# Optimization experiments

Measured on AMD Instinct MI355X. Metric: run time of the kernel, lower is better.

Reference implementation:

```python
import jax, jax.numpy as jnp
import numpy as np

B, L, H, U = 4, 4096, 1024, 1024


def setup_inputs() -> dict:
    key = jax.random.key(0)
    k0, k1, k2, k3 = jax.random.split(key, 4)
    inputs = jax.random.normal(k0, (B, L, H), dtype=jnp.float32)
    # linear layer params (torch default init scale ~ 1/sqrt(fan_in))
    W_rkv = jax.random.normal(k1, (H, 3 * U), dtype=jnp.float32) / np.sqrt(H)
    b_rkv = jnp.zeros((3 * U,), dtype=jnp.float32)
    W_o = jax.random.normal(k2, (U, H), dtype=jnp.float32) / np.sqrt(U)
    b_o = jnp.zeros((H,), dtype=jnp.float32)
    # nu_log init exactly as in the torch module
    r_min, r_max = 0.9, 0.999
    u = jax.random.uniform(k3, (U,), dtype=jnp.float32)
    nu_log = jnp.log(-0.5 * jnp.log(u * (r_max ** 2 - r_min ** 2) + r_min ** 2))
    gamma_log = jnp.zeros((U,), dtype=jnp.float32)
    return {"inputs": inputs, "W_rkv": W_rkv, "b_rkv": b_rkv,
            "W_o": W_o, "b_o": b_o, "nu_log": nu_log, "gamma_log": gamma_log}


def reference(inputs, W_rkv, b_rkv, W_o, b_o, nu_log, gamma_log):
    # projections
    rkv = jnp.einsum('blh,hu->blu', inputs, W_rkv) + b_rkv  # [B,L,3U]
    r, k, v = jnp.split(rkv, 3, axis=-1)
    r = jax.nn.sigmoid(r)
    k = jnp.exp(k)
    kv = k * v
    u = jnp.concatenate([kv, k], axis=-1)                   # [B,L,2U]
    nu = jnp.exp(jnp.concatenate([nu_log, nu_log]))         # [2U]
    gamma = jnp.exp(nu_log + gamma_log) - 1.0               # [U]
    lam = jnp.exp(-nu)                                      # per-channel decay
    # The torch log-depth doubling scan computes the linear recurrence
    # y_t = lam * y_{t-1} + u_t (y_0 = u_0). Use an associative scan over L.
    a = jnp.broadcast_to(lam, u.shape)

    def combine(c1, c2):
        a1, x1 = c1
        a2, x2 = c2
        return (a1 * a2, x1 * a2 + x2)

    _, y = jax.lax.associative_scan(combine, (a, u), axis=1)  # [B,L,2U]
    u1, u2 = jnp.split(y, 2, axis=-1)
    x = (u1 + gamma * kv) / (u2 + gamma * k + 1e-6) * r       # [B,L,U]
    return jnp.einsum('blu,uh->blh', x, W_o) + b_o
```

## Files before the change

kernel.cpp:

```cpp
#include <hip/hip_runtime.h>
#include <hip/hip_bf16.h>
#include <cstdint>
#include <cstddef>

constexpr int NB = 4;
constexpr int NL = 4096;
constexpr int NH = 1024;
constexpr int NU = 1024;
constexpr int NM = NB * NL;
constexpr int NCHUNK = 32;
constexpr int CLEN = NL / NCHUNK;

typedef __bf16 bf16x8 __attribute__((ext_vector_type(8)));
typedef __bf16 bf16x4 __attribute__((ext_vector_type(4)));
typedef float  f32x4  __attribute__((ext_vector_type(4)));

__global__ __launch_bounds__(256) void cast_f32_to_bf16(
    const float* __restrict__ in, __bf16* __restrict__ out, int n4) {
  int stride = gridDim.x * 256;
  for (int i = blockIdx.x * 256 + threadIdx.x; i < n4; i += stride) {
    const float4 v = reinterpret_cast<const float4*>(in)[i];
    bf16x4 o;
    o[0] = (__bf16)v.x; o[1] = (__bf16)v.y; o[2] = (__bf16)v.z; o[3] = (__bf16)v.w;
    reinterpret_cast<bf16x4*>(out)[i] = o;
  }
}

__global__ __launch_bounds__(256) void transpose_cast(
    const float* __restrict__ W, __bf16* __restrict__ Wt, int K, int N) {
  __shared__ float tile[32][33];
  int tx = threadIdx.x, ty = threadIdx.y;
  int n0 = blockIdx.x * 32, k0 = blockIdx.y * 32;
  #pragma unroll
  for (int i = 0; i < 32; i += 8)
    tile[ty + i][tx] = W[(size_t)(k0 + ty + i) * N + n0 + tx];
  __syncthreads();
  #pragma unroll
  for (int i = 0; i < 32; i += 8)
    Wt[(size_t)(n0 + ty + i) * K + k0 + tx] = (__bf16)tile[tx][ty + i];
}


#define SBAR0 __builtin_amdgcn_sched_barrier(0)

template<int EPI>
__global__ __launch_bounds__(512, 2) void gemm256(
    const __bf16* __restrict__ A, const __bf16* __restrict__ Bt,
    int M, int N, int K,
    const float* __restrict__ bias,
    float* __restrict__ out_r, float* __restrict__ out_k, float* __restrict__ out_v,
    float* __restrict__ out_f32) {
  __shared__ __attribute__((aligned(16))) __bf16 sA[2][256 * 64];
  __shared__ __attribute__((aligned(16))) __bf16 sB[2][256 * 64];

  const int tid = threadIdx.x;
  const int lane = tid & 63;
  const int w = tid >> 6;
  const int wm = w >> 2, wn = w & 3;

  const int ntn = N >> 8;
  const int nwg = gridDim.x;
  const int bid = blockIdx.x;
  const int cpx = nwg >> 3;
  const int swz = (bid & 7) * cpx + (bid >> 3);
  const int mt = swz / ntn, nt = swz % ntn;
  const long m0 = (long)mt * 256;
  const long n0 = (long)nt * 256;
  const int KT = K >> 6;

  const int srow = lane >> 3;
  const int scol = ((lane & 7) ^ srow) << 4;

  auto stageA = [&](int bi, int qm, int t) {
    if (t >= KT) return;
    #pragma unroll
    for (int j = 0; j < 2; ++j) {
      int u = w * 2 + j;
      int row0 = (u < 8) ? (qm * 64 + u * 8) : (128 + qm * 64 + (u - 8) * 8);
      const char* src = (const char*)A + ((m0 + row0 + srow) * (long)K + (long)t * 64) * 2 + scol;
      __builtin_amdgcn_global_load_lds(
          (const __attribute__((address_space(1))) unsigned int*)src,
          (__attribute__((address_space(3))) unsigned int*)((char*)&sA[bi][0] + row0 * 128),
          16, 0, 0);
    }
  };
  auto stageB = [&](int bi, int qn, int t) {
    if (t >= KT) return;
    #pragma unroll
    for (int j = 0; j < 2; ++j) {
      int u = w * 2 + j;
      int row0 = (u >> 2) * 64 + qn * 32 + (u & 3) * 8;
      const char* src = (const char*)Bt + ((n0 + row0 + srow) * (long)K + (long)t * 64) * 2 + scol;
      __builtin_amdgcn_global_load_lds(
          (const __attribute__((address_space(1))) unsigned int*)src,
          (__attribute__((address_space(3))) unsigned int*)((char*)&sB[bi][0] + row0 * 128),
          16, 0, 0);
    }
  };

  f32x4 acc[8][4];
  #pragma unroll
  for (int i = 0; i < 8; ++i)
    #pragma unroll
    for (int j = 0; j < 4; ++j) acc[i][j] = (f32x4)0.f;

#define PHASE(QM, QN, STAGE_STMT)                                              \
  do {                                                                         \
    const char* sAb = (const char*)&sA[bi][0];                                 \
    const char* sBb = (const char*)&sB[bi][0];                                 \
    bf16x8 av[4][2], bv[2][2];                                                 \
    _Pragma("unroll")                                                          \
    for (int f = 0; f < 4; ++f) {                                              \
      _Pragma("unroll")                                                        \
      for (int ks = 0; ks < 2; ++ks) {                                         \
        int r = wm * 128 + ((QM) * 4 + f) * 16 + (lane & 15);                  \
        int c = ks * 64 + (lane & 48);                                         \
        av[f][ks] = *(const bf16x8*)(sAb + r * 128 + (c ^ ((r & 7) << 4)));    \
      }                                                                        \
    }                                                                          \
    _Pragma("unroll")                                                          \
    for (int g = 0; g < 2; ++g) {                                              \
      _Pragma("unroll")                                                        \
      for (int ks = 0; ks < 2; ++ks) {                                         \
        int r = wn * 64 + ((QN) * 2 + g) * 16 + (lane & 15);                   \
        int c = ks * 64 + (lane & 48);                                         \
        bv[g][ks] = *(const bf16x8*)(sBb + r * 128 + (c ^ ((r & 7) << 4)));    \
      }                                                                        \
    }                                                                          \
    STAGE_STMT;                                                                \
    SBAR0;                                                                     \
    __builtin_amdgcn_s_barrier();                                              \
    SBAR0;                                                                     \
    __builtin_amdgcn_s_setprio(1);                                             \
    _Pragma("unroll")                                                          \
    for (int f = 0; f < 4; ++f) {                                              \
      _Pragma("unroll")                                                        \
      for (int g = 0; g < 2; ++g) {                                            \
        acc[(QM) * 4 + f][(QN) * 2 + g] = __builtin_amdgcn_mfma_f32_16x16x32_bf16( \
            av[f][0], bv[g][0], acc[(QM) * 4 + f][(QN) * 2 + g], 0, 0, 0);     \
        acc[(QM) * 4 + f][(QN) * 2 + g] = __builtin_amdgcn_mfma_f32_16x16x32_bf16( \
            av[f][1], bv[g][1], acc[(QM) * 4 + f][(QN) * 2 + g], 0, 0, 0);     \
      }                                                                        \
    }                                                                          \
    __builtin_amdgcn_s_setprio(0);                                             \
    SBAR0;                                                                     \
  } while (0)

#define EBAR { __builtin_amdgcn_s_barrier(); SBAR0; }

  stageA(0, 0, 0); stageB(0, 0, 0); stageA(0, 1, 0); stageB(0, 1, 0);
  stageA(1, 0, 1); stageB(1, 0, 1);
  SBAR0;
  asm volatile("s_waitcnt vmcnt(4)" ::: "memory");
  EBAR;

  for (int t = 0; t < KT; ++t) {
    const int bi = t & 1;
    PHASE(0, 0, stageB(bi ^ 1, 1, t + 1)); EBAR;
    PHASE(1, 0, stageA(bi ^ 1, 1, t + 1)); EBAR;
    PHASE(0, 1, stageB(bi, 0, t + 2));     EBAR;
    PHASE(1, 1, stageA(bi, 0, t + 2));
    SBAR0;
    if (t < KT - 2) { asm volatile("s_waitcnt vmcnt(4)" ::: "memory"); }
    else            { asm volatile("s_waitcnt vmcnt(0)" ::: "memory"); }
    EBAR;
  }
#undef PHASE
#undef EBAR

  float bs[4];
  #pragma unroll
  for (int fn = 0; fn < 4; ++fn)
    bs[fn] = bias[n0 + wn * 64 + fn * 16 + (lane & 15)];

  #pragma unroll
  for (int fm = 0; fm < 8; ++fm) {
    #pragma unroll
    for (int fn = 0; fn < 4; ++fn) {
      #pragma unroll
      for (int rr = 0; rr < 4; ++rr) {
        long row = m0 + wm * 128 + fm * 16 + (lane >> 4) * 4 + rr;
        long col = n0 + wn * 64 + fn * 16 + (lane & 15);
        float val = acc[fm][fn][rr] + bs[fn];
        if constexpr (EPI == 0) {
          int reg = (int)(col >> 10);
          int u = (int)(col & 1023);
          size_t idx = (size_t)row * NU + u;
          if (reg == 0)      out_r[idx] = 1.f / (1.f + __expf(-val));
          else if (reg == 1) out_k[idx] = __expf(val);
          else               out_v[idx] = val;
        } else {
          out_f32[(size_t)row * N + col] = val;
        }
      }
    }
  }
}

__global__ __launch_bounds__(256) void scan_pass1(
    const float* __restrict__ kbuf, const float* __restrict__ vbuf,
    const float* __restrict__ nu_log,
    float* __restrict__ S1, float* __restrict__ S2) {
  int u = blockIdx.x * 256 + threadIdx.x;
  int c = blockIdx.y;
  int b = blockIdx.z;
  float lam = __expf(-__expf(nu_log[u]));
  size_t base = ((size_t)b * NL + (size_t)c * CLEN) * NU + u;
  float y1 = 0.f, y2 = 0.f;
  #pragma unroll 4
  for (int t = 0; t < CLEN; ++t) {
    float kk = kbuf[base + (size_t)t * NU];
    float vv = vbuf[base + (size_t)t * NU];
    y1 = fmaf(lam, y1, kk * vv);
    y2 = fmaf(lam, y2, kk);
  }
  size_t si = ((size_t)b * NCHUNK + c) * NU + u;
  S1[si] = y1;
  S2[si] = y2;
}

__global__ __launch_bounds__(256) void scan_combine(
    const float* __restrict__ S1, const float* __restrict__ S2,
    const float* __restrict__ nu_log,
    float* __restrict__ C1, float* __restrict__ C2) {
  int u = blockIdx.x * 256 + threadIdx.x;
  int b = blockIdx.y;
  float lamCL = __expf(-__expf(nu_log[u]) * (float)CLEN);
  float y1 = 0.f, y2 = 0.f;
  for (int c = 0; c < NCHUNK; ++c) {
    size_t si = ((size_t)b * NCHUNK + c) * NU + u;
    C1[si] = y1;
    C2[si] = y2;
    y1 = fmaf(lamCL, y1, S1[si]);
    y2 = fmaf(lamCL, y2, S2[si]);
  }
}

__global__ __launch_bounds__(256) void scan_pass2(
    const float* __restrict__ kbuf, const float* __restrict__ vbuf,
    const float* __restrict__ rbuf,
    const float* __restrict__ C1, const float* __restrict__ C2,
    const float* __restrict__ nu_log, const float* __restrict__ gamma_log,
    __bf16* __restrict__ xbuf) {
  int u = blockIdx.x * 256 + threadIdx.x;
  int c = blockIdx.y;
  int b = blockIdx.z;
  float lam = __expf(-__expf(nu_log[u]));
  float gamma = __expf(nu_log[u] + gamma_log[u]) - 1.f;
  size_t si = ((size_t)b * NCHUNK + c) * NU + u;
  float y1 = C1[si], y2 = C2[si];
  size_t base = ((size_t)b * NL + (size_t)c * CLEN) * NU + u;
  #pragma unroll 4
  for (int t = 0; t < CLEN; ++t) {
    size_t idx = base + (size_t)t * NU;
    float kk = kbuf[idx];
    float vv = vbuf[idx];
    float rr = rbuf[idx];
    float kv = kk * vv;
    y1 = fmaf(lam, y1, kv);
    y2 = fmaf(lam, y2, kk);
    float x = (y1 + gamma * kv) / (y2 + gamma * kk + 1e-6f) * rr;
    xbuf[idx] = (__bf16)x;
  }
}

extern "C" void kernel_launch(void* const* d_in, const int* in_sizes, int n_in,
                              void* d_out, int out_size, void* d_ws, size_t ws_size,
                              hipStream_t stream) {
  const float* inputs    = (const float*)d_in[0];
  const float* W_rkv     = (const float*)d_in[1];
  const float* b_rkv     = (const float*)d_in[2];
  const float* W_o       = (const float*)d_in[3];
  const float* b_o       = (const float*)d_in[4];
  const float* nu_log    = (const float*)d_in[5];
  const float* gamma_log = (const float*)d_in[6];
  float* out = (float*)d_out;

  char* ws = (char*)d_ws;
  size_t off = 0;
  __bf16* Abuf  = (__bf16*)(ws + off); off += (size_t)NM * NH * 2;
  __bf16* WrkvT = (__bf16*)(ws + off); off += (size_t)3 * NU * NH * 2;
  __bf16* WoT   = (__bf16*)(ws + off); off += (size_t)NH * NU * 2;
  float*  rbuf  = (float*)(ws + off);  off += (size_t)NM * NU * 4;
  float*  kbuf  = (float*)(ws + off);  off += (size_t)NM * NU * 4;
  float*  vbuf  = (float*)(ws + off);  off += (size_t)NM * NU * 4;
  float*  S1    = (float*)(ws + off);  off += (size_t)NB * NCHUNK * NU * 4;
  float*  S2    = (float*)(ws + off);  off += (size_t)NB * NCHUNK * NU * 4;
  float*  C1    = (float*)(ws + off);  off += (size_t)NB * NCHUNK * NU * 4;
  float*  C2    = (float*)(ws + off);  off += (size_t)NB * NCHUNK * NU * 4;
  __bf16* xbuf  = Abuf;

  cast_f32_to_bf16<<<2048, 256, 0, stream>>>(inputs, Abuf, (NM * NH) / 4);

  transpose_cast<<<dim3(3 * NU / 32, NH / 32), dim3(32, 8), 0, stream>>>(W_rkv, WrkvT, NH, 3 * NU);
  transpose_cast<<<dim3(NH / 32, NU / 32), dim3(32, 8), 0, stream>>>(W_o, WoT, NU, NH);

  gemm256<0><<<(NM / 256) * (3 * NU / 256), 512, 0, stream>>>(
      Abuf, WrkvT, NM, 3 * NU, NH, b_rkv, rbuf, kbuf, vbuf, nullptr);

  scan_pass1<<<dim3(NU / 256, NCHUNK, NB), 256, 0, stream>>>(kbuf, vbuf, nu_log, S1, S2);
  scan_combine<<<dim3(NU / 256, NB), 256, 0, stream>>>(S1, S2, nu_log, C1, C2);
  scan_pass2<<<dim3(NU / 256, NCHUNK, NB), 256, 0, stream>>>(
      kbuf, vbuf, rbuf, C1, C2, nu_log, gamma_log, xbuf);

  gemm256<1><<<(NM / 256) * (NH / 256), 512, 0, stream>>>(
      xbuf, WoT, NM, NH, NU, b_o, nullptr, nullptr, nullptr, out);
}
```

Measured before the change: 368.1 us.

## Store r/k/v intermediates in bf16, restructure GEMM fragment reuse, double scan chunks

The projection GEMM epilogue now writes r, k and v as bf16 instead of fp32, halving the intermediate traffic written by the GEMM and read by both scan passes. The GEMM main loop is reorganised so A and B fragments loaded from LDS are reused across quadrants rather than reloaded each phase, and the prologue waits on all loads. The scan uses twice as many chunks for more parallelism in the scan passes. Storing exp(k) in bf16 loses precision in the ratio, which risks accuracy.

```diff
diff --git a/kernel.cpp b/kernel.cpp
--- a/kernel.cpp
+++ b/kernel.cpp
@@ -8,7 +8,7 @@
 constexpr int NH = 1024;
 constexpr int NU = 1024;
 constexpr int NM = NB * NL;
-constexpr int NCHUNK = 32;
+constexpr int NCHUNK = 64;
 constexpr int CLEN = NL / NCHUNK;
 
 typedef __bf16 bf16x8 __attribute__((ext_vector_type(8)));
@@ -48,7 +48,7 @@
     const __bf16* __restrict__ A, const __bf16* __restrict__ Bt,
     int M, int N, int K,
     const float* __restrict__ bias,
-    float* __restrict__ out_r, float* __restrict__ out_k, float* __restrict__ out_v,
+    __bf16* __restrict__ out_r, __bf16* __restrict__ out_k, __bf16* __restrict__ out_v,
     float* __restrict__ out_f32) {
   __shared__ __attribute__((aligned(16))) __bf16 sA[2][256 * 64];
   __shared__ __attribute__((aligned(16))) __bf16 sB[2][256 * 64];
@@ -104,68 +104,74 @@
     #pragma unroll
     for (int j = 0; j < 4; ++j) acc[i][j] = (f32x4)0.f;
 
-#define PHASE(QM, QN, STAGE_STMT)                                              \
-  do {                                                                         \
-    const char* sAb = (const char*)&sA[bi][0];                                 \
-    const char* sBb = (const char*)&sB[bi][0];                                 \
-    bf16x8 av[4][2], bv[2][2];                                                 \
+  bf16x8 a0[4][2], a1[4][2], bb[2][2];
+
+#define LDA(DST, QM)                                                           \
+  _Pragma("unroll")                                                            \
+  for (int f = 0; f < 4; ++f) {                                                \
     _Pragma("unroll")                                                          \
-    for (int f = 0; f < 4; ++f) {                                              \
-      _Pragma("unroll")                                                        \
-      for (int ks = 0; ks < 2; ++ks) {                                         \
-        int r = wm * 128 + ((QM) * 4 + f) * 16 + (lane & 15);                  \
-        int c = ks * 64 + (lane & 48);                                         \
-        av[f][ks] = *(const bf16x8*)(sAb + r * 128 + (c ^ ((r & 7) << 4)));    \
-      }                                                                        \
+    for (int ks = 0; ks < 2; ++ks) {                                           \
+      int r = wm * 128 + ((QM) * 4 + f) * 16 + (lane & 15);                    \
+      int c = ks * 64 + (lane & 48);                                           \
+      DST[f][ks] = *(const bf16x8*)(sAb + r * 128 + (c ^ ((r & 7) << 4)));     \
     }                                                                          \
+  }
+#define LDB(DST, QN)                                                           \
+  _Pragma("unroll")                                                            \
+  for (int g = 0; g < 2; ++g) {                                                \
+    _Pragma("unroll")                                                          \
+    for (int ks = 0; ks < 2; ++ks) {                                           \
+      int r = wn * 64 + ((QN) * 2 + g) * 16 + (lane & 15);                     \
+      int c = ks * 64 + (lane & 48);                                           \
+      DST[g][ks] = *(const bf16x8*)(sBb + r * 128 + (c ^ ((r & 7) << 4)));     \
+    }                                                                          \
+  }
+#define MFMAQ(QM, QN, AV, BV)                                                  \
+  __builtin_amdgcn_s_setprio(1);                                               \
+  _Pragma("unroll")                                                            \
+  for (int f = 0; f < 4; ++f) {                                                \
     _Pragma("unroll")                                                          \
     for (int g = 0; g < 2; ++g) {                                              \
-      _Pragma("unroll")                                                        \
-      for (int ks = 0; ks < 2; ++ks) {                                         \
-        int r = wn * 64 + ((QN) * 2 + g) * 16 + (lane & 15);                   \
-        int c = ks * 64 + (lane & 48);                                         \
-        bv[g][ks] = *(const bf16x8*)(sBb + r * 128 + (c ^ ((r & 7) << 4)));    \
-      }                                                                        \
+      acc[(QM) * 4 + f][(QN) * 2 + g] = __builtin_amdgcn_mfma_f32_16x16x32_bf16( \
+          AV[f][0], BV[g][0], acc[(QM) * 4 + f][(QN) * 2 + g], 0, 0, 0);       \
+      acc[(QM) * 4 + f][(QN) * 2 + g] = __builtin_amdgcn_mfma_f32_16x16x32_bf16( \
+          AV[f][1], BV[g][1], acc[(QM) * 4 + f][(QN) * 2 + g], 0, 0, 0);       \
     }                                                                          \
-    STAGE_STMT;                                                                \
-    SBAR0;                                                                     \
-    __builtin_amdgcn_s_barrier();                                              \
-    SBAR0;                                                                     \
-    __builtin_amdgcn_s_setprio(1);                                             \
-    _Pragma("unroll")                                                          \
-    for (int f = 0; f < 4; ++f) {                                              \
-      _Pragma("unroll")                                                        \
-      for (int g = 0; g < 2; ++g) {                                            \
-        acc[(QM) * 4 + f][(QN) * 2 + g] = __builtin_amdgcn_mfma_f32_16x16x32_bf16( \
-            av[f][0], bv[g][0], acc[(QM) * 4 + f][(QN) * 2 + g], 0, 0, 0);     \
-        acc[(QM) * 4 + f][(QN) * 2 + g] = __builtin_amdgcn_mfma_f32_16x16x32_bf16( \
-            av[f][1], bv[g][1], acc[(QM) * 4 + f][(QN) * 2 + g], 0, 0, 0);     \
-      }                                                                        \
-    }                                                                          \
-    __builtin_amdgcn_s_setprio(0);                                             \
-    SBAR0;                                                                     \
-  } while (0)
-
+  }                                                                            \
+  __builtin_amdgcn_s_setprio(0);
+#define PBAR { SBAR0; __builtin_amdgcn_s_barrier(); SBAR0; }
 #define EBAR { __builtin_amdgcn_s_barrier(); SBAR0; }
 
-  stageA(0, 0, 0); stageB(0, 0, 0); stageA(0, 1, 0); stageB(0, 1, 0);
-  stageA(1, 0, 1); stageB(1, 0, 1);
-  SBAR0;
-  asm volatile("s_waitcnt vmcnt(4)" ::: "memory");
+  stageA(0, 0, 0); SBAR0;
+  stageB(0, 0, 0); SBAR0;
+  stageA(0, 1, 0); SBAR0;
+  stageB(0, 1, 0); SBAR0;
+  stageA(1, 0, 1); SBAR0;
+  stageB(1, 0, 1); SBAR0;
+  asm volatile("s_waitcnt vmcnt(0)" ::: "memory");
   EBAR;
 
   for (int t = 0; t < KT; ++t) {
     const int bi = t & 1;
-    PHASE(0, 0, stageB(bi ^ 1, 1, t + 1)); EBAR;
-    PHASE(1, 0, stageA(bi ^ 1, 1, t + 1)); EBAR;
-    PHASE(0, 1, stageB(bi, 0, t + 2));     EBAR;
-    PHASE(1, 1, stageA(bi, 0, t + 2));
+    const char* sAb = (const char*)&sA[bi][0];
+    const char* sBb = (const char*)&sB[bi][0];
+    LDA(a0, 0); LDB(bb, 0); stageB(bi ^ 1, 1, t + 1);
+    PBAR; MFMAQ(0, 0, a0, bb); SBAR0; EBAR;
+    LDA(a1, 1); stageA(bi ^ 1, 1, t + 1);
+    PBAR; MFMAQ(1, 0, a1, bb); SBAR0; EBAR;
+    LDB(bb, 1); stageB(bi, 0, t + 2);
+    PBAR; MFMAQ(0, 1, a0, bb); SBAR0; EBAR;
+    stageA(bi, 0, t + 2);
+    PBAR; MFMAQ(1, 1, a1, bb); SBAR0;
     SBAR0;
     if (t < KT - 2) { asm volatile("s_waitcnt vmcnt(4)" ::: "memory"); }
     else            { asm volatile("s_waitcnt vmcnt(0)" ::: "memory"); }
     EBAR;
   }
-#undef PHASE
+#undef LDA
+#undef LDB
+#undef MFMAQ
+#undef PBAR
 #undef EBAR
 
   float bs[4];
@@ -186,9 +192,9 @@
           int reg = (int)(col >> 10);
           int u = (int)(col & 1023);
           size_t idx = (size_t)row * NU + u;
-          if (reg == 0)      out_r[idx] = 1.f / (1.f + __expf(-val));
-          else if (reg == 1) out_k[idx] = __expf(val);
-          else               out_v[idx] = val;
+          if (reg == 0)      out_r[idx] = (__bf16)(1.f / (1.f + __expf(-val)));
+          else if (reg == 1) out_k[idx] = (__bf16)__expf(val);
+          else               out_v[idx] = (__bf16)val;
         } else {
           out_f32[(size_t)row * N + col] = val;
         }
@@ -198,7 +204,7 @@
 }
 
 __global__ __launch_bounds__(256) void scan_pass1(
-    const float* __restrict__ kbuf, const float* __restrict__ vbuf,
+    const __bf16* __restrict__ kbuf, const __bf16* __restrict__ vbuf,
     const float* __restrict__ nu_log,
     float* __restrict__ S1, float* __restrict__ S2) {
   int u = blockIdx.x * 256 + threadIdx.x;
@@ -209,8 +215,8 @@
   float y1 = 0.f, y2 = 0.f;
   #pragma unroll 4
   for (int t = 0; t < CLEN; ++t) {
-    float kk = kbuf[base + (size_t)t * NU];
-    float vv = vbuf[base + (size_t)t * NU];
+    float kk = (float)kbuf[base + (size_t)t * NU];
+    float vv = (float)vbuf[base + (size_t)t * NU];
     y1 = fmaf(lam, y1, kk * vv);
     y2 = fmaf(lam, y2, kk);
   }
@@ -237,8 +243,8 @@
 }
 
 __global__ __launch_bounds__(256) void scan_pass2(
-    const float* __restrict__ kbuf, const float* __restrict__ vbuf,
-    const float* __restrict__ rbuf,
+    const __bf16* __restrict__ kbuf, const __bf16* __restrict__ vbuf,
+    const __bf16* __restrict__ rbuf,
     const float* __restrict__ C1, const float* __restrict__ C2,
     const float* __restrict__ nu_log, const float* __restrict__ gamma_log,
     __bf16* __restrict__ xbuf) {
@@ -253,9 +259,9 @@
   #pragma unroll 4
   for (int t = 0; t < CLEN; ++t) {
     size_t idx = base + (size_t)t * NU;
-    float kk = kbuf[idx];
-    float vv = vbuf[idx];
-    float rr = rbuf[idx];
+    float kk = (float)kbuf[idx];
+    float vv = (float)vbuf[idx];
+    float rr = (float)rbuf[idx];
     float kv = kk * vv;
     y1 = fmaf(lam, y1, kv);
     y2 = fmaf(lam, y2, kk);
@@ -281,9 +287,9 @@
   __bf16* Abuf  = (__bf16*)(ws + off); off += (size_t)NM * NH * 2;
   __bf16* WrkvT = (__bf16*)(ws + off); off += (size_t)3 * NU * NH * 2;
   __bf16* WoT   = (__bf16*)(ws + off); off += (size_t)NH * NU * 2;
-  float*  rbuf  = (float*)(ws + off);  off += (size_t)NM * NU * 4;
-  float*  kbuf  = (float*)(ws + off);  off += (size_t)NM * NU * 4;
-  float*  vbuf  = (float*)(ws + off);  off += (size_t)NM * NU * 4;
+  __bf16* rbuf  = (__bf16*)(ws + off); off += (size_t)NM * NU * 2;
+  __bf16* kbuf  = (__bf16*)(ws + off); off += (size_t)NM * NU * 2;
+  __bf16* vbuf  = (__bf16*)(ws + off); off += (size_t)NM * NU * 2;
   float*  S1    = (float*)(ws + off);  off += (size_t)NB * NCHUNK * NU * 4;
   float*  S2    = (float*)(ws + off);  off += (size_t)NB * NCHUNK * NU * 4;
   float*  C1    = (float*)(ws + off);  off += (size_t)NB * NCHUNK * NU * 4;
```

Measured after the change: 345.5 us. 1.07x faster.
